# Kernel optimization log

Measured on AMD Instinct MI355X. Metric: run time of the kernel, lower is better.

## Reference

```python
import jax, jax.numpy as jnp
import numpy as np

FULL_SCALE = 128
TOPK = 8
R = 0.5


def setup_inputs() -> dict:
    key = jax.random.key(0)
    ks = jax.random.split(key, 6)
    B, Na, Nb, D = 4, 8192, 8192, 256
    return {
        "a_feats": jax.random.normal(ks[0], (B, Na, D), jnp.float32),
        "b_feats": jax.random.normal(ks[1], (B, Nb, D), jnp.float32),
        "coords_a": jax.random.randint(ks[2], (B, Na, 3), 0, 2048, jnp.int32),
        "coords_b": jax.random.randint(ks[3], (B, Nb, 3), 0, 2048, jnp.int32),
        "w1": jax.random.normal(ks[4], (D, 2 * D), jnp.float32) / np.sqrt(2 * D),
        "b1": jnp.zeros((D,), jnp.float32),
        "w2": jax.random.normal(ks[5], (D, D), jnp.float32) / np.sqrt(D),
        "b2": jnp.zeros((D,), jnp.float32),
    }


def _cli_one(af, bf, ca, cb, w1, b1, w2, b2):
    # af:[Na,D] bf:[Nb,D] ca:[Na,3] cb:[Nb,3] (float coords, already //16)
    # torch.cdist (euclidean) / full_scale
    d2 = (jnp.sum(ca * ca, 1)[:, None] + jnp.sum(cb * cb, 1)[None, :]
          - 2.0 * ca @ cb.T)
    dist = jnp.sqrt(jnp.maximum(d2, 0.0)) / FULL_SCALE  # [Na, Nb]
    neg_d, idx = jax.lax.top_k(-dist, TOPK)             # smallest k distances
    dw = R - jnp.clip(-neg_d, 0.0, R)                   # [Na, k]
    nb = bf[idx]                                        # gather [Na, k, D]
    x = jnp.concatenate([nb, af[:, None, :] - nb], axis=-1)  # [Na, k, 2D]
    h = jax.nn.relu(jnp.einsum('nkf,df->nkd', x, w1) + b1) * dw[..., None]
    o = jnp.einsum('nkd,ed->nke', h, w2) + b2           # [Na, k, D]
    return jnp.sum(o, axis=1)                           # [Na, D]


def reference(a_feats, b_feats, coords_a, coords_b, w1, b1, w2, b2):
    ca = (coords_a // 16).astype(jnp.float32)
    cb = (coords_b // 16).astype(jnp.float32)
    fuse = jax.vmap(lambda af, bf, x, y: _cli_one(af, bf, x, y, w1, b1, w2, b2))(
        a_feats, b_feats, ca, cb)
    # ME.cat(a, tmp): concatenate features along channel dim
    return jnp.concatenate([a_feats, fuse], axis=-1)  # [B, Na, 2D]
```

## Files before the change

kernel.cpp:

```cpp
#include <hip/hip_runtime.h>
#include <math.h>

typedef short short8_t __attribute__((ext_vector_type(8)));
typedef __bf16 bf16x8_t __attribute__((ext_vector_type(8)));
typedef float f32x4_t __attribute__((ext_vector_type(4)));

__device__ __forceinline__ float bf2f(unsigned short u) {
  unsigned v = ((unsigned)u) << 16;
  return __builtin_bit_cast(float, v);
}
__device__ __forceinline__ unsigned short f2bf(float f) {
  unsigned x = __builtin_bit_cast(unsigned, f);
  x += 0x7fffu + ((x >> 16) & 1u);
  return (unsigned short)(x >> 16);
}

#define NA 8192
#define NB 8192
#define NBATCH 4
#define DIM 256
#define NPTS (NBATCH * NA)
#define NCELL 2048
#define SUBL 8

__device__ __forceinline__ void kins(unsigned k[8], unsigned x) {
  unsigned c = x < k[7] ? x : k[7];
#pragma unroll
  for (int i = 6; i >= 0; i--) {
    unsigned hi = k[i] > c ? k[i] : c;
    c = k[i] < c ? k[i] : c;
    k[i + 1] = hi;
  }
  k[0] = c;
}

__global__ __launch_bounds__(256) void prep_weights(
    const float* __restrict__ w1, const float* __restrict__ w2,
    unsigned short* __restrict__ Wdiff, unsigned short* __restrict__ Wb,
    unsigned short* __restrict__ W2b) {
  int d = blockIdx.x, t = threadIdx.x;
  float wa = w1[d * 512 + t];
  float wb = w1[d * 512 + 256 + t];
  Wdiff[d * 256 + t] = f2bf(wa - wb);
  Wb[d * 256 + t] = f2bf(wb);
  W2b[d * 256 + t] = f2bf(w2[d * 256 + t]);
}

__global__ __launch_bounds__(256) void cvt_f32_bf16(
    const float* __restrict__ in, unsigned short* __restrict__ out) {
  size_t i = (size_t)(blockIdx.x * 256 + threadIdx.x) * 4;
  float4 v = *(const float4*)(in + i);
  ushort4 o;
  o.x = f2bf(v.x); o.y = f2bf(v.y); o.z = f2bf(v.z); o.w = f2bf(v.w);
  *(ushort4*)(out + i) = o;
}

__global__ __launch_bounds__(256) void zero_counts(
    unsigned* __restrict__ bcnt, unsigned* __restrict__ acnt,
    unsigned* __restrict__ failcnt) {
  int i = blockIdx.x * 256 + threadIdx.x;
  bcnt[i] = 0;
  acnt[i] = 0;
  if (i == 0) *failcnt = 0;
}

__global__ __launch_bounds__(256) void pack_count(
    const int* __restrict__ coords, unsigned* __restrict__ pk,
    unsigned* __restrict__ cnt) {
  int i = blockIdx.x * 256 + threadIdx.x;
  int x = (coords[(size_t)i * 3 + 0] >> 4) & 127;
  int y = (coords[(size_t)i * 3 + 1] >> 4) & 127;
  int z = (coords[(size_t)i * 3 + 2] >> 4) & 127;
  pk[i] = (unsigned)(x | (y << 7) | (z << 14));
  int cid = ((i >> 13) << 9) | ((x >> 4) << 6) | ((y >> 4) << 3) | (z >> 4);
  atomicAdd(cnt + cid, 1u);
}

__global__ __launch_bounds__(256) void scan_cells(
    const unsigned* __restrict__ bcnt, const unsigned* __restrict__ acnt,
    unsigned* __restrict__ boff, unsigned* __restrict__ aoff,
    unsigned* __restrict__ bcur, unsigned* __restrict__ acur) {
  __shared__ unsigned p[256];
  const int t = threadIdx.x;
  for (int tab = 0; tab < 2; tab++) {
    const unsigned* cnt = tab ? acnt : bcnt;
    unsigned* off = tab ? aoff : boff;
    unsigned* cur = tab ? acur : bcur;
    unsigned loc[8], sum = 0;
#pragma unroll
    for (int k = 0; k < 8; k++) { loc[k] = sum; sum += cnt[t * 8 + k]; }
    p[t] = sum;
    __syncthreads();
    for (int d = 1; d < 256; d <<= 1) {
      unsigned v = (t >= d) ? p[t - d] : 0u;
      __syncthreads();
      p[t] += v;
      __syncthreads();
    }
    unsigned base = (t == 0) ? 0u : p[t - 1];
#pragma unroll
    for (int k = 0; k < 8; k++) {
      unsigned o = base + loc[k];
      off[t * 8 + k] = o;
      cur[t * 8 + k] = o;
    }
    if (t == 255) off[2048] = base + sum;
    __syncthreads();
  }
}

__global__ __launch_bounds__(256) void scatter_pts(
    const unsigned* __restrict__ pk, unsigned* __restrict__ cur,
    uint2* __restrict__ out) {
  int i = blockIdx.x * 256 + threadIdx.x;
  unsigned v = pk[i];
  int cx = (v & 127) >> 4, cy = ((v >> 7) & 127) >> 4, cz = ((v >> 14) & 127) >> 4;
  int cid = ((i >> 13) << 9) | (cx << 6) | (cy << 3) | cz;
  unsigned pos = atomicAdd(cur + cid, 1u);
  out[pos] = make_uint2(v, (unsigned)(i & 8191));
}

#define LDT 72
__global__ __launch_bounds__(256) void gemm_bf16(
    const short* __restrict__ A, const short* __restrict__ W,
    float* __restrict__ Cf, unsigned short* __restrict__ Cb,
    const float* __restrict__ bias, float bias_scale,
    int c_stride, int c_coloff) {
  __shared__ __attribute__((aligned(16))) short As[128 * LDT];
  __shared__ __attribute__((aligned(16))) short Bs[128 * LDT];
  const int tid = threadIdx.x;
  const int row0 = blockIdx.x * 128;
  const int col0 = blockIdx.y * 128;
  const int w = tid >> 6, lane = tid & 63;
  const int wm = (w & 1) * 64, wn = (w >> 1) * 64;
  f32x4_t acc[4][4] = {};
  for (int k0 = 0; k0 < 256; k0 += 64) {
#pragma unroll
    for (int i = 0; i < 4; i++) {
      int c = tid + 256 * i;
      int r = c >> 3, kc = (c & 7) * 8;
      short8_t va = *(const short8_t*)(A + (size_t)(row0 + r) * 256 + k0 + kc);
      *(short8_t*)(As + r * LDT + kc) = va;
      short8_t vb = *(const short8_t*)(W + (size_t)(col0 + r) * 256 + k0 + kc);
      *(short8_t*)(Bs + r * LDT + kc) = vb;
    }
    __syncthreads();
#pragma unroll
    for (int kk = 0; kk < 64; kk += 32) {
      const int kof = kk + (lane >> 4) * 8;
      bf16x8_t af[4], bfr[4];
#pragma unroll
      for (int i = 0; i < 4; i++) {
        af[i] = __builtin_bit_cast(bf16x8_t,
            *(const short8_t*)(As + (wm + i * 16 + (lane & 15)) * LDT + kof));
        bfr[i] = __builtin_bit_cast(bf16x8_t,
            *(const short8_t*)(Bs + (wn + i * 16 + (lane & 15)) * LDT + kof));
      }
#pragma unroll
      for (int i = 0; i < 4; i++)
#pragma unroll
        for (int j = 0; j < 4; j++)
          acc[i][j] = __builtin_amdgcn_mfma_f32_16x16x32_bf16(
              af[i], bfr[j], acc[i][j], 0, 0, 0);
    }
    __syncthreads();
  }
#pragma unroll
  for (int i = 0; i < 4; i++) {
    int row = row0 + wm + i * 16 + ((lane >> 4) * 4);
#pragma unroll
    for (int j = 0; j < 4; j++) {
      int col = col0 + wn + j * 16 + (lane & 15);
      float bv = bias ? bias[col] * bias_scale : 0.f;
#pragma unroll
      for (int r = 0; r < 4; r++) {
        float v = acc[i][j][r] + bv;
        size_t off = (size_t)(row + r) * c_stride + c_coloff + col;
        if (Cf) Cf[off] = v;
        else Cb[off] = f2bf(v);
      }
    }
  }
}

__global__ __launch_bounds__(256) void topk_bins(
    const unsigned* __restrict__ boff, const uint2* __restrict__ bcj,
    const uint2* __restrict__ acj, int* __restrict__ idxb,
    float* __restrict__ dwb, unsigned* __restrict__ failcnt,
    unsigned* __restrict__ faillist) {
  const int tid = blockIdx.x * 256 + threadIdx.x;
  const int t = tid / SUBL;
  const int sub = tid & (SUBL - 1);
  const uint2 av = acj[t];
  const int batch = t >> 13;
  const int ax = av.x & 127, ay = (av.x >> 7) & 127, az = (av.x >> 14) & 127;
  const int cx = ax >> 4, cy = ay >> 4, cz = az >> 4;
  const int xlo = max(cx - 1, 0), xhi = min(cx + 1, 7);
  const int ylo = max(cy - 1, 0), yhi = min(cy + 1, 7);
  const int zlo = max(cz - 1, 0), zhi1 = min(cz + 1, 7) + 1;
  unsigned k[8];
#pragma unroll
  for (int s = 0; s < 8; s++) k[s] = 0xFFFFFFF8u + s;
  for (int nx = xlo; nx <= xhi; nx++) {
    for (int ny = ylo; ny <= yhi; ny++) {
      const int cb = (batch << 9) | (nx << 6) | (ny << 3);
      const int gs = (int)boff[cb + zlo];
      const int ge = (int)boff[cb + zhi1];
      for (int i = gs + sub; i < ge; i += SUBL) {
        const uint2 b = bcj[i];
        const int dx = ax - (int)(b.x & 127);
        const int dy = ay - (int)((b.x >> 7) & 127);
        const int dz = az - (int)((b.x >> 14) & 127);
        const unsigned d2 = (unsigned)(__mul24(dx, dx) + __mul24(dy, dy) +
                                       __mul24(dz, dz));
        kins(k, (d2 << 13) | b.y);
      }
    }
  }
  const int lane = threadIdx.x & 63;
#pragma unroll
  for (int half = 1; half < SUBL; half <<= 1) {
    unsigned o[8];
#pragma unroll
    for (int s = 0; s < 8; s++)
      o[s] = (unsigned)__shfl((int)k[s], lane ^ half, 64);
#pragma unroll
    for (int s = 0; s < 8; s++) kins(k, o[s]);
  }
  if (sub == 0) {
    const int g = (batch << 13) | (int)av.y;
#pragma unroll
    for (int s = 0; s < 8; s++) {
      unsigned key = k[s];
      idxb[(size_t)g * 8 + s] = (int)(key & 8191u);
      float dist = sqrtf((float)(key >> 13)) * (1.0f / 128.0f);
      dwb[(size_t)g * 8 + s] = 0.5f - fminf(dist, 0.5f);
    }
    if (k[7] >= (289u << 13)) {
      unsigned fp = atomicAdd(failcnt, 1u);
      faillist[fp] = (unsigned)g;
    }
  }
}

__global__ __launch_bounds__(256) void topk_fallback(
    const unsigned* __restrict__ failcnt, const unsigned* __restrict__ faillist,
    const uint2* __restrict__ bcj, const unsigned* __restrict__ apk,
    int* __restrict__ idxb, float* __restrict__ dwb) {
  __shared__ unsigned sk[4 * 8];
  const int tid = threadIdx.x;
  const int wv = tid >> 6, lane = tid & 63;
  const unsigned nf = *failcnt;
  for (unsigned fi = blockIdx.x; fi < nf; fi += gridDim.x) {
    const unsigned g = faillist[fi];
    const int batch = (int)(g >> 13);
    const unsigned av = apk[g];
    const int ax = av & 127, ay = (av >> 7) & 127, az = (av >> 14) & 127;
    const uint2* pb = bcj + ((size_t)batch << 13);
    unsigned k[8];
#pragma unroll
    for (int s = 0; s < 8; s++) k[s] = 0xFFFFFFF8u + s;
#pragma unroll 8
    for (int i = tid; i < NB; i += 256) {
      const uint2 b = pb[i];
      const int dx = ax - (int)(b.x & 127);
      const int dy = ay - (int)((b.x >> 7) & 127);
      const int dz = az - (int)((b.x >> 14) & 127);
      const unsigned d2 = (unsigned)(__mul24(dx, dx) + __mul24(dy, dy) +
                                     __mul24(dz, dz));
      kins(k, (d2 << 13) | b.y);
    }
#pragma unroll
    for (int half = 32; half >= 1; half >>= 1) {
      unsigned o[8];
#pragma unroll
      for (int s = 0; s < 8; s++)
        o[s] = (unsigned)__shfl((int)k[s], lane ^ half, 64);
#pragma unroll
      for (int s = 0; s < 8; s++) kins(k, o[s]);
    }
    if (lane == 0) {
#pragma unroll
      for (int s = 0; s < 8; s++) sk[wv * 8 + s] = k[s];
    }
    __syncthreads();
    if (tid == 0) {
#pragma unroll
      for (int w = 1; w < 4; w++)
#pragma unroll
        for (int s = 0; s < 8; s++) kins(k, sk[w * 8 + s]);
#pragma unroll
      for (int s = 0; s < 8; s++) {
        unsigned key = k[s];
        idxb[(size_t)g * 8 + s] = (int)(key & 8191u);
        float dist = sqrtf((float)(key >> 13)) * (1.0f / 128.0f);
        dwb[(size_t)g * 8 + s] = 0.5f - fminf(dist, 0.5f);
      }
    }
    __syncthreads();
  }
}

__global__ __launch_bounds__(256) void fuse_kernel(
    const unsigned short* __restrict__ Pa, const unsigned short* __restrict__ Pb,
    const int* __restrict__ idxb, const float* __restrict__ dwb,
    const float* __restrict__ a_feats, unsigned short* __restrict__ H,
    float* __restrict__ outp) {
  const int g = blockIdx.x * 4 + (threadIdx.x >> 6);
  const int lane = threadIdx.x & 63;
  const int batch = g >> 13;
  const size_t fo = (size_t)g * 256 + lane * 4;
  ushort4 pav = *(const ushort4*)(Pa + fo);
  const float pa0 = bf2f(pav.x), pa1 = bf2f(pav.y), pa2 = bf2f(pav.z),
              pa3 = bf2f(pav.w);
  float h0 = 0.f, h1 = 0.f, h2 = 0.f, h3 = 0.f;
  const size_t bbase = (size_t)(batch << 13) * 256;
#pragma unroll
  for (int k = 0; k < 8; k++) {
    const int j = idxb[(size_t)g * 8 + k];
    const float w = dwb[(size_t)g * 8 + k];
    const ushort4 pbv =
        *(const ushort4*)(Pb + bbase + (size_t)j * 256 + lane * 4);
    h0 += fmaxf(pa0 + bf2f(pbv.x), 0.f) * w;
    h1 += fmaxf(pa1 + bf2f(pbv.y), 0.f) * w;
    h2 += fmaxf(pa2 + bf2f(pbv.z), 0.f) * w;
    h3 += fmaxf(pa3 + bf2f(pbv.w), 0.f) * w;
  }
  ushort4 hv;
  hv.x = f2bf(h0); hv.y = f2bf(h1); hv.z = f2bf(h2); hv.w = f2bf(h3);
  *(ushort4*)(H + fo) = hv;
  float4 av = *(const float4*)(a_feats + fo);
  *(float4*)(outp + (size_t)g * 512 + lane * 4) = av;
}

extern "C" void kernel_launch(void* const* d_in, const int* in_sizes, int n_in,
                              void* d_out, int out_size, void* d_ws,
                              size_t ws_size, hipStream_t stream) {
  const float* a_feats = (const float*)d_in[0];
  const float* b_feats = (const float*)d_in[1];
  const int* coords_a = (const int*)d_in[2];
  const int* coords_b = (const int*)d_in[3];
  const float* w1 = (const float*)d_in[4];
  const float* b1 = (const float*)d_in[5];
  const float* w2 = (const float*)d_in[6];
  const float* b2 = (const float*)d_in[7];
  float* outp = (float*)d_out;

  char* p = (char*)d_ws;
  auto take = [&](size_t bytes) {
    char* r = p;
    p += (bytes + 255) & ~(size_t)255;
    return r;
  };
  unsigned short* Ab = (unsigned short*)take((size_t)NPTS * DIM * 2);
  unsigned short* Bb = (unsigned short*)take((size_t)NPTS * DIM * 2);
  unsigned short* Pa = (unsigned short*)take((size_t)NPTS * DIM * 2);
  unsigned short* Pb = (unsigned short*)take((size_t)NPTS * DIM * 2);
  unsigned short* Hb = (unsigned short*)take((size_t)NPTS * DIM * 2);
  int* idxb = (int*)take((size_t)NPTS * 8 * 4);
  float* dwb = (float*)take((size_t)NPTS * 8 * 4);
  unsigned* bpk = (unsigned*)take((size_t)NPTS * 4);
  unsigned* apk = (unsigned*)take((size_t)NPTS * 4);
  unsigned* bcnt = (unsigned*)take(NCELL * 4);
  unsigned* acnt = (unsigned*)take(NCELL * 4);
  unsigned* bcur = (unsigned*)take(NCELL * 4);
  unsigned* acur = (unsigned*)take(NCELL * 4);
  unsigned* boff = (unsigned*)take((NCELL + 1) * 4);
  unsigned* aoff = (unsigned*)take((NCELL + 1) * 4);
  uint2* bcj = (uint2*)take((size_t)NPTS * 8);
  uint2* acj = (uint2*)take((size_t)NPTS * 8);
  unsigned* failcnt = (unsigned*)take(256);
  unsigned* faillist = (unsigned*)take((size_t)NPTS * 4);
  unsigned short* Wdiff = (unsigned short*)take(256 * 256 * 2);
  unsigned short* Wb16 = (unsigned short*)take(256 * 256 * 2);
  unsigned short* W2b = (unsigned short*)take(256 * 256 * 2);

  prep_weights<<<256, 256, 0, stream>>>(w1, w2, Wdiff, Wb16, W2b);
  cvt_f32_bf16<<<NPTS * DIM / 1024, 256, 0, stream>>>(a_feats, Ab);
  cvt_f32_bf16<<<NPTS * DIM / 1024, 256, 0, stream>>>(b_feats, Bb);

  zero_counts<<<NCELL / 256, 256, 0, stream>>>(bcnt, acnt, failcnt);
  pack_count<<<NPTS / 256, 256, 0, stream>>>(coords_b, bpk, bcnt);
  pack_count<<<NPTS / 256, 256, 0, stream>>>(coords_a, apk, acnt);
  scan_cells<<<1, 256, 0, stream>>>(bcnt, acnt, boff, aoff, bcur, acur);
  scatter_pts<<<NPTS / 256, 256, 0, stream>>>(bpk, bcur, bcj);
  scatter_pts<<<NPTS / 256, 256, 0, stream>>>(apk, acur, acj);

  gemm_bf16<<<dim3(NPTS / 128, 2), 256, 0, stream>>>(
      (const short*)Ab, (const short*)Wb16, nullptr, Pa, b1, 1.0f, 256, 0);
  gemm_bf16<<<dim3(NPTS / 128, 2), 256, 0, stream>>>(
      (const short*)Bb, (const short*)Wdiff, nullptr, Pb, nullptr, 0.0f, 256, 0);

  topk_bins<<<NPTS * SUBL / 256, 256, 0, stream>>>(boff, bcj, acj, idxb, dwb,
                                                   failcnt, faillist);
  topk_fallback<<<256, 256, 0, stream>>>(failcnt, faillist, bcj, apk, idxb,
                                         dwb);

  fuse_kernel<<<NPTS / 4, 256, 0, stream>>>(Pa, Pb, idxb, dwb, a_feats, Hb,
                                            outp);

  gemm_bf16<<<dim3(NPTS / 128, 2), 256, 0, stream>>>(
      (const short*)Hb, (const short*)W2b, outp, nullptr, b2, 8.0f, 512, 256);
}
```

Measured before the change: 250.7 us.

## Fuse fp32-to-bf16 conversion and a_feats copy into full-width GEMM

Removes the two standalone f32-to-bf16 conversion kernels. The GEMMs now read fp32 activations directly and convert them while staging into shared memory. The first GEMM also writes a_feats into the left half of the output, so fuse_kernel no longer does that copy. The GEMM becomes 512-thread blocks that each cover all 256 output columns, which reads A once instead of twice. This cuts memory traffic and launch count, at the cost of halving the grid and doubling the B tile in LDS, which may lower occupancy.

```diff
diff --git a/kernel.cpp b/kernel.cpp
--- a/kernel.cpp
+++ b/kernel.cpp
@@ -44,15 +44,6 @@
   Wdiff[d * 256 + t] = f2bf(wa - wb);
   Wb[d * 256 + t] = f2bf(wb);
   W2b[d * 256 + t] = f2bf(w2[d * 256 + t]);
-}
-
-__global__ __launch_bounds__(256) void cvt_f32_bf16(
-    const float* __restrict__ in, unsigned short* __restrict__ out) {
-  size_t i = (size_t)(blockIdx.x * 256 + threadIdx.x) * 4;
-  float4 v = *(const float4*)(in + i);
-  ushort4 o;
-  o.x = f2bf(v.x); o.y = f2bf(v.y); o.z = f2bf(v.z); o.w = f2bf(v.w);
-  *(ushort4*)(out + i) = o;
 }
 
 __global__ __launch_bounds__(256) void zero_counts(
@@ -121,28 +112,57 @@
 }
 
 #define LDT 72
-__global__ __launch_bounds__(256) void gemm_bf16(
-    const short* __restrict__ A, const short* __restrict__ W,
+template <int F32IN>
+__global__ __launch_bounds__(512) void gemm_wide(
+    const void* __restrict__ Ain, const short* __restrict__ W,
     float* __restrict__ Cf, unsigned short* __restrict__ Cb,
     const float* __restrict__ bias, float bias_scale,
-    int c_stride, int c_coloff) {
+    int c_stride, int c_coloff, float* __restrict__ copyout) {
   __shared__ __attribute__((aligned(16))) short As[128 * LDT];
-  __shared__ __attribute__((aligned(16))) short Bs[128 * LDT];
+  __shared__ __attribute__((aligned(16))) short Bs[256 * LDT];
   const int tid = threadIdx.x;
   const int row0 = blockIdx.x * 128;
-  const int col0 = blockIdx.y * 128;
   const int w = tid >> 6, lane = tid & 63;
   const int wm = (w & 1) * 64, wn = (w >> 1) * 64;
   f32x4_t acc[4][4] = {};
   for (int k0 = 0; k0 < 256; k0 += 64) {
+    if (F32IN) {
+      const float* Af = (const float*)Ain;
+#pragma unroll
+      for (int i = 0; i < 2; i++) {
+        int c = tid + 512 * i;
+        int r = c >> 3, kc = (c & 7) * 8;
+        const float* src = Af + (size_t)(row0 + r) * 256 + k0 + kc;
+        float4 v0 = *(const float4*)src;
+        float4 v1 = *(const float4*)(src + 4);
+        short8_t vb;
+        vb[0] = (short)f2bf(v0.x); vb[1] = (short)f2bf(v0.y);
+        vb[2] = (short)f2bf(v0.z); vb[3] = (short)f2bf(v0.w);
+        vb[4] = (short)f2bf(v1.x); vb[5] = (short)f2bf(v1.y);
+        vb[6] = (short)f2bf(v1.z); vb[7] = (short)f2bf(v1.w);
+        *(short8_t*)(As + r * LDT + kc) = vb;
+        if (copyout) {
+          float4* dst = (float4*)(copyout + (size_t)(row0 + r) * 512 + k0 + kc);
+          dst[0] = v0;
+          dst[1] = v1;
+        }
+      }
+    } else {
+      const short* Ab = (const short*)Ain;
+#pragma unroll
+      for (int i = 0; i < 2; i++) {
+        int c = tid + 512 * i;
+        int r = c >> 3, kc = (c & 7) * 8;
+        *(short8_t*)(As + r * LDT + kc) =
+            *(const short8_t*)(Ab + (size_t)(row0 + r) * 256 + k0 + kc);
+      }
+    }
 #pragma unroll
     for (int i = 0; i < 4; i++) {
-      int c = tid + 256 * i;
+      int c = tid + 512 * i;
       int r = c >> 3, kc = (c & 7) * 8;
-      short8_t va = *(const short8_t*)(A + (size_t)(row0 + r) * 256 + k0 + kc);
-      *(short8_t*)(As + r * LDT + kc) = va;
-      short8_t vb = *(const short8_t*)(W + (size_t)(col0 + r) * 256 + k0 + kc);
-      *(short8_t*)(Bs + r * LDT + kc) = vb;
+      *(short8_t*)(Bs + r * LDT + kc) =
+          *(const short8_t*)(W + (size_t)r * 256 + k0 + kc);
     }
     __syncthreads();
 #pragma unroll
@@ -170,7 +190,7 @@
     int row = row0 + wm + i * 16 + ((lane >> 4) * 4);
 #pragma unroll
     for (int j = 0; j < 4; j++) {
-      int col = col0 + wn + j * 16 + (lane & 15);
+      int col = wn + j * 16 + (lane & 15);
       float bv = bias ? bias[col] * bias_scale : 0.f;
 #pragma unroll
       for (int r = 0; r < 4; r++) {
@@ -304,8 +324,7 @@
 __global__ __launch_bounds__(256) void fuse_kernel(
     const unsigned short* __restrict__ Pa, const unsigned short* __restrict__ Pb,
     const int* __restrict__ idxb, const float* __restrict__ dwb,
-    const float* __restrict__ a_feats, unsigned short* __restrict__ H,
-    float* __restrict__ outp) {
+    unsigned short* __restrict__ H) {
   const int g = blockIdx.x * 4 + (threadIdx.x >> 6);
   const int lane = threadIdx.x & 63;
   const int batch = g >> 13;
@@ -329,8 +348,6 @@
   ushort4 hv;
   hv.x = f2bf(h0); hv.y = f2bf(h1); hv.z = f2bf(h2); hv.w = f2bf(h3);
   *(ushort4*)(H + fo) = hv;
-  float4 av = *(const float4*)(a_feats + fo);
-  *(float4*)(outp + (size_t)g * 512 + lane * 4) = av;
 }
 
 extern "C" void kernel_launch(void* const* d_in, const int* in_sizes, int n_in,
@@ -352,8 +369,6 @@
     p += (bytes + 255) & ~(size_t)255;
     return r;
   };
-  unsigned short* Ab = (unsigned short*)take((size_t)NPTS * DIM * 2);
-  unsigned short* Bb = (unsigned short*)take((size_t)NPTS * DIM * 2);
   unsigned short* Pa = (unsigned short*)take((size_t)NPTS * DIM * 2);
   unsigned short* Pb = (unsigned short*)take((size_t)NPTS * DIM * 2);
   unsigned short* Hb = (unsigned short*)take((size_t)NPTS * DIM * 2);
@@ -376,8 +391,6 @@
   unsigned short* W2b = (unsigned short*)take(256 * 256 * 2);
 
   prep_weights<<<256, 256, 0, stream>>>(w1, w2, Wdiff, Wb16, W2b);
-  cvt_f32_bf16<<<NPTS * DIM / 1024, 256, 0, stream>>>(a_feats, Ab);
-  cvt_f32_bf16<<<NPTS * DIM / 1024, 256, 0, stream>>>(b_feats, Bb);
 
   zero_counts<<<NCELL / 256, 256, 0, stream>>>(bcnt, acnt, failcnt);
   pack_count<<<NPTS / 256, 256, 0, stream>>>(coords_b, bpk, bcnt);
@@ -386,19 +399,21 @@
   scatter_pts<<<NPTS / 256, 256, 0, stream>>>(bpk, bcur, bcj);
   scatter_pts<<<NPTS / 256, 256, 0, stream>>>(apk, acur, acj);
 
-  gemm_bf16<<<dim3(NPTS / 128, 2), 256, 0, stream>>>(
-      (const short*)Ab, (const short*)Wb16, nullptr, Pa, b1, 1.0f, 256, 0);
-  gemm_bf16<<<dim3(NPTS / 128, 2), 256, 0, stream>>>(
-      (const short*)Bb, (const short*)Wdiff, nullptr, Pb, nullptr, 0.0f, 256, 0);
+  gemm_wide<1><<<NPTS / 128, 512, 0, stream>>>(
+      (const void*)a_feats, (const short*)Wb16, nullptr, Pa, b1, 1.0f, 256, 0,
+      outp);
+  gemm_wide<1><<<NPTS / 128, 512, 0, stream>>>(
+      (const void*)b_feats, (const short*)Wdiff, nullptr, Pb, nullptr, 0.0f,
+      256, 0, nullptr);
 
   topk_bins<<<NPTS * SUBL / 256, 256, 0, stream>>>(boff, bcj, acj, idxb, dwb,
                                                    failcnt, faillist);
   topk_fallback<<<256, 256, 0, stream>>>(failcnt, faillist, bcj, apk, idxb,
                                          dwb);
 
-  fuse_kernel<<<NPTS / 4, 256, 0, stream>>>(Pa, Pb, idxb, dwb, a_feats, Hb,
-                                            outp);
-
-  gemm_bf16<<<dim3(NPTS / 128, 2), 256, 0, stream>>>(
-      (const short*)Hb, (const short*)W2b, outp, nullptr, b2, 8.0f, 512, 256);
-}
+  fuse_kernel<<<NPTS / 4, 256, 0, stream>>>(Pa, Pb, idxb, dwb, Hb);
+
+  gemm_wide<0><<<NPTS / 128, 512, 0, stream>>>(
+      (const void*)Hb, (const short*)W2b, outp, nullptr, b2, 8.0f, 512, 256,
+      nullptr);
+}
```

New measurement: 246.2 us. About the same (-1.8%).
